# Performance work log

Hardware: AMD Instinct MI355X
Metric: run time of the kernel (lower is better)

Reference implementation:

```python
import jax, jax.numpy as jnp
import numpy as np

B = 32768
MAXD = 60               # max raw feature dim (user)
DIMS = [60, 51, 43]     # user, event, space
H = 256                 # HIDDEN_DIM
E = 256                 # EMBED_DIM
NH = 4                  # num heads
HD = H // NH            # head dim = 64
SCALE = float(np.sqrt(HD))
EPS = 1e-5


def setup_inputs() -> dict:
    key = jax.random.key(0)
    ks = iter(jax.random.split(key, 64))
    def rn(shape, scale=0.05):
        return jax.random.normal(next(ks), shape, dtype=jnp.float32) * scale
    inp = {}
    inp["anchor_feats"] = jax.random.normal(next(ks), (B, MAXD), dtype=jnp.float32)
    inp["item_feats"] = jax.random.normal(next(ks), (B, MAXD), dtype=jnp.float32)
    inp["anchor_type_ids"] = jax.random.randint(next(ks), (B,), 0, 3, dtype=jnp.int32)
    inp["item_type_ids"] = jax.random.randint(next(ks), (B,), 0, 3, dtype=jnp.int32)
    # per-type encoder MLPs; W1 zero-padded beyond each type's input dim (matches torch slicing x[:, :dim])
    W1 = rn((3, MAXD, H))
    row_mask = np.zeros((3, MAXD, 1), dtype=np.float32)
    for t, d in enumerate(DIMS):
        row_mask[t, :d, 0] = 1.0
    inp["enc_W1"] = W1 * jnp.asarray(row_mask)
    inp["enc_b1"] = rn((3, H)); inp["enc_g1"] = jnp.ones((3, H)); inp["enc_be1"] = jnp.zeros((3, H))
    inp["enc_W2"] = rn((3, H, H))
    inp["enc_b2"] = rn((3, H)); inp["enc_g2"] = jnp.ones((3, H)); inp["enc_be2"] = jnp.zeros((3, H))
    # two stacked HGT layers; 9 edge types (src*3+dst), 3 node types
    inp["hgt_Wk"] = rn((2, 9, H, H)); inp["hgt_Wq"] = rn((2, 9, H, H)); inp["hgt_Wv"] = rn((2, 9, H, H))
    inp["hgt_Wout"] = rn((2, 3, H, H))
    inp["hgt_g"] = jnp.ones((2, 3, H)); inp["hgt_b"] = jnp.zeros((2, 3, H))
    inp["out_W"] = rn((H, E)); inp["out_b"] = rn((E,))
    inp["out_g"] = jnp.ones((E,)); inp["out_be"] = jnp.zeros((E,))
    return inp


def _ln(x, g, b):
    m = x.mean(-1, keepdims=True)
    v = ((x - m) ** 2).mean(-1, keepdims=True)
    return (x - m) / jnp.sqrt(v + EPS) * g + b


def _encode(feats, tids, W1, b1, g1, be1, W2, b2, g2, be2):
    # per-type 2-layer MLP (Linear->LN->ReLU x2, dropout=eval noop), masked select
    h = jnp.zeros((feats.shape[0], H), feats.dtype)
    for t in range(3):
        z = jax.nn.relu(_ln(feats @ W1[t] + b1[t], g1[t], be1[t]))
        z = jax.nn.relu(_ln(z @ W2[t] + b2[t], g2[t], be2[t]))
        h = jnp.where((tids == t)[:, None], z, h)
    return h


def _hgt_apply(Wk, Wq, Wv, Wout, g, b, e, dt, src_h, dst_h):
    # single-dim dot-product attention per head, sigmoid gate
    Bn = src_h.shape[0]
    k = (src_h @ Wk[e]).reshape(Bn, NH, HD)
    q = (dst_h @ Wq[e]).reshape(Bn, NH, HD)
    v = (src_h @ Wv[e]).reshape(Bn, NH, HD)
    attn = jax.nn.sigmoid((q * k).sum(-1, keepdims=True) / SCALE)
    msg = (attn * v).reshape(Bn, H)
    return _ln(dst_h + msg @ Wout[dt], g[dt], b[dt])


def _hgt_hop(Wk, Wq, Wv, Wout, g, b, ha, hi, atid, itid):
    # torch code: ha_out from clone of ha, hi updated per disjoint (atype,itype) mask,
    # both updates read ORIGINAL ha/hi for each masked element
    ha_new, hi_new = ha, hi
    for a in range(3):
        for i in range(3):
            mask = ((atid == a) & (itid == i))[:, None]
            ua = _hgt_apply(Wk, Wq, Wv, Wout, g, b, i * 3 + a, a, hi, ha)  # item -> anchor
            ui = _hgt_apply(Wk, Wq, Wv, Wout, g, b, a * 3 + i, i, ha, hi)  # anchor -> item
            ha_new = jnp.where(mask, ua, ha_new)
            hi_new = jnp.where(mask, ui, hi_new)
    return ha_new, hi_new


def _l2norm(x):
    return x / jnp.maximum(jnp.linalg.norm(x, axis=-1, keepdims=True), 1e-12)


def reference(anchor_feats, item_feats, anchor_type_ids, item_type_ids,
              enc_W1, enc_b1, enc_g1, enc_be1, enc_W2, enc_b2, enc_g2, enc_be2,
              hgt_Wk, hgt_Wq, hgt_Wv, hgt_Wout, hgt_g, hgt_b,
              out_W, out_b, out_g, out_be):
    ha = _encode(anchor_feats, anchor_type_ids, enc_W1, enc_b1, enc_g1, enc_be1, enc_W2, enc_b2, enc_g2, enc_be2)
    hi = _encode(item_feats, item_type_ids, enc_W1, enc_b1, enc_g1, enc_be1, enc_W2, enc_b2, enc_g2, enc_be2)
    for L in range(2):
        ha, hi = _hgt_hop(hgt_Wk[L], hgt_Wq[L], hgt_Wv[L], hgt_Wout[L], hgt_g[L], hgt_b[L],
                          ha, hi, anchor_type_ids, item_type_ids)
    anchor_emb = _l2norm(_ln(ha @ out_W + out_b, out_g, out_be))
    item_emb = _l2norm(_ln(hi @ out_W + out_b, out_g, out_be))
    return anchor_emb, item_emb
```

## Files before the change

### kernel.cpp

```cpp
#include <hip/hip_runtime.h>
#include <math.h>

#define BN   32768
#define MAXD 60
#define HDIM 256
#define TR   16
#define LDX  260

typedef __attribute__((ext_vector_type(4))) float f32x4;
typedef __attribute__((ext_vector_type(8))) short bf16x8;

#define MFMA(a, b, c) __builtin_amdgcn_mfma_f32_16x16x32_bf16(a, b, c, 0, 0, 0)

__device__ __forceinline__ unsigned short f2bf(float f) {
  union { float f; unsigned u; } v; v.f = f;
  unsigned r = v.u + 0x7FFF + ((v.u >> 16) & 1);
  return (unsigned short)(r >> 16);
}

template <int LDXE>
__device__ __forceinline__ bf16x8 ldsAx(const unsigned short* buf, int rf,
                                        int ks, int lane) {
  const int row = rf * 16 + (lane & 15);
  const int ko = ks * 32 + ((lane >> 4) << 3);
  return *(const bf16x8*)(buf + row * LDXE + ko);
}

template <int KS>
__device__ __forceinline__ bf16x8 fragB(const unsigned short* __restrict__ W,
                                        int cfw, int ks, int lane) {
  return *(const bf16x8*)(W + ((size_t)(cfw * KS + ks) << 9) + (lane << 3));
}

__device__ __forceinline__ float red16(float p) {
  p += __shfl_xor(p, 1); p += __shfl_xor(p, 2);
  p += __shfl_xor(p, 4); p += __shfl_xor(p, 8);
  return p;
}

__device__ __forceinline__ void cross_ln(float* redS, float* redQ,
                                         const float sums[2][4],
                                         const float sumq[2][4], int lane,
                                         int wid, float mo[2][4],
                                         float ro[2][4]) {
  __syncthreads();
  if ((lane & 15) == 0) {
    #pragma unroll
    for (int rf = 0; rf < 2; ++rf)
      #pragma unroll
      for (int rr = 0; rr < 4; ++rr) {
        const int row = rf * 16 + ((lane >> 4) << 2) + rr;
        redS[row * 4 + wid] = sums[rf][rr];
        redQ[row * 4 + wid] = sumq[rf][rr];
      }
  }
  __syncthreads();
  #pragma unroll
  for (int rf = 0; rf < 2; ++rf)
    #pragma unroll
    for (int rr = 0; rr < 4; ++rr) {
      const int row = rf * 16 + ((lane >> 4) << 2) + rr;
      float s = redS[row * 4] + redS[row * 4 + 1] + redS[row * 4 + 2] + redS[row * 4 + 3];
      float z = redQ[row * 4] + redQ[row * 4 + 1] + redQ[row * 4 + 2] + redQ[row * 4 + 3];
      float m = s * (1.0f / HDIM);
      mo[rf][rr] = m;
      ro[rf][rr] = rsqrtf(z * (1.0f / HDIM) - m * m + 1e-5f);
    }
}


__device__ __forceinline__ void row_reduce(float* red, const float acc[TR],
                                           float m[TR], float rs[TR], int j) {
  const int lane = j & 63, wv = j >> 6;
  __syncthreads();
  #pragma unroll
  for (int r = 0; r < TR; ++r) {
    float s = acc[r], q = acc[r] * acc[r];
    #pragma unroll
    for (int o = 32; o; o >>= 1) { s += __shfl_xor(s, o); q += __shfl_xor(q, o); }
    if (lane == 0) { red[r * 8 + wv * 2] = s; red[r * 8 + wv * 2 + 1] = q; }
  }
  __syncthreads();
  #pragma unroll
  for (int r = 0; r < TR; ++r) {
    float s = red[r * 8 + 0] + red[r * 8 + 2] + red[r * 8 + 4] + red[r * 8 + 6];
    float q = red[r * 8 + 1] + red[r * 8 + 3] + red[r * 8 + 5] + red[r * 8 + 7];
    float mean = s * (1.0f / HDIM);
    float var  = q * (1.0f / HDIM) - mean * mean;
    m[r]  = mean;
    rs[r] = rsqrtf(var + 1e-5f);
  }
}

template <int KD, int ST>
__device__ __forceinline__ void matvec_l(const float* __restrict__ W,
                                         const float* zz, float acc[TR], int j) {
  #pragma unroll 2
  for (int k = 0; k < KD; k += 4) {
    const float w0 = W[(k + 0) * HDIM + j];
    const float w1 = W[(k + 1) * HDIM + j];
    const float w2 = W[(k + 2) * HDIM + j];
    const float w3 = W[(k + 3) * HDIM + j];
    #pragma unroll
    for (int r = 0; r < TR; ++r) {
      const float4 x = *(const float4*)(zz + r * ST + k);
      acc[r] = fmaf(x.w, w3, fmaf(x.z, w2, fmaf(x.y, w1, fmaf(x.x, w0, acc[r]))));
    }
  }
}


__global__ __launch_bounds__(256) void bucket_kernel(
    const int* __restrict__ atid, const int* __restrict__ itid,
    int* cnts, int* idxA, int* idxI, int* idxC) {
  __shared__ int lcnt[15], lbase[15];
  const int tid = threadIdx.x;
  const int r = blockIdx.x * 256 + tid;
  if (tid < 15) lcnt[tid] = 0;
  __syncthreads();
  const int a = atid[r], i = itid[r];
  const int c = a * 3 + i;
// ... 100 lines not shown
    const int col = (wid << 6) + (cf << 4) + (lane & 15);
    cb[cf] = b1[t * HDIM + col]; cg[cf] = g1[t * HDIM + col]; cbe[cf] = be1[t * HDIM + col];
  }
  float sums[2][4] = {}, sumq[2][4] = {};
  #pragma unroll
  for (int rf = 0; rf < 2; ++rf)
    #pragma unroll
    for (int cf = 0; cf < 4; ++cf)
      #pragma unroll
      for (int rr = 0; rr < 4; ++rr) {
        float x = acc[rf][cf][rr] + cb[cf];
        acc[rf][cf][rr] = x;
        sums[rf][rr] += x; sumq[rf][rr] += x * x;
      }
  #pragma unroll
  for (int rf = 0; rf < 2; ++rf)
    #pragma unroll
    for (int rr = 0; rr < 4; ++rr) { sums[rf][rr] = red16(sums[rf][rr]); sumq[rf][rr] = red16(sumq[rf][rr]); }
  float m[2][4], rs[2][4];
  cross_ln(sm.redS, sm.redQ, sums, sumq, lane, wid, m, rs);
  #pragma unroll
  for (int rf = 0; rf < 2; ++rf)
    #pragma unroll
    for (int cf = 0; cf < 4; ++cf) {
      const int col = (wid << 6) + (cf << 4) + (lane & 15);
      #pragma unroll
      for (int rr = 0; rr < 4; ++rr) {
        const int row = rf * 16 + ((lane >> 4) << 2) + rr;
        float zz = fmaxf((acc[rf][cf][rr] - m[rf][rr]) * rs[rf][rr] * cg[cf] + cbe[cf], 0.0f);
        sm.z[row * LDX + col] = f2bf(zz);
      }
    }
  __syncthreads();

  #pragma unroll
  for (int rf = 0; rf < 2; ++rf)
    #pragma unroll
    for (int cf = 0; cf < 4; ++cf) acc[rf][cf] = (f32x4){0.f, 0.f, 0.f, 0.f};
  #pragma unroll 2
  for (int ks = 0; ks < 8; ++ks) {
    bf16x8 a0 = ldsAx<LDX>(sm.z, 0, ks, lane);
    bf16x8 a1 = ldsAx<LDX>(sm.z, 1, ks, lane);
    #pragma unroll
    for (int cf = 0; cf < 4; ++cf) {
      bf16x8 w = fragB<8>(pW2 + (size_t)t * 65536, (wid << 2) + cf, ks, lane);
      acc[0][cf] = MFMA(a0, w, acc[0][cf]);
      acc[1][cf] = MFMA(a1, w, acc[1][cf]);
    }
  }
  #pragma unroll
  for (int cf = 0; cf < 4; ++cf) {
    const int col = (wid << 6) + (cf << 4) + (lane & 15);
    cb[cf] = b2[t * HDIM + col]; cg[cf] = g2[t * HDIM + col]; cbe[cf] = be2[t * HDIM + col];
  }
  float sums2[2][4] = {}, sumq2[2][4] = {};
  #pragma unroll
  for (int rf = 0; rf < 2; ++rf)
    #pragma unroll
    for (int cf = 0; cf < 4; ++cf)
      #pragma unroll
      for (int rr = 0; rr < 4; ++rr) {
        float x = acc[rf][cf][rr] + cb[cf];
        acc[rf][cf][rr] = x;
        sums2[rf][rr] += x; sumq2[rf][rr] += x * x;
      }
  #pragma unroll
  for (int rf = 0; rf < 2; ++rf)
    #pragma unroll
    for (int rr = 0; rr < 4; ++rr) { sums2[rf][rr] = red16(sums2[rf][rr]); sumq2[rf][rr] = red16(sumq2[rf][rr]); }
  cross_ln(sm.redS, sm.redQ, sums2, sumq2, lane, wid, m, rs);
  #pragma unroll
  for (int rf = 0; rf < 2; ++rf)
    #pragma unroll
    for (int cf = 0; cf < 4; ++cf) {
      const int col = (wid << 6) + (cf << 4) + (lane & 15);
      #pragma unroll
      for (int rr = 0; rr < 4; ++rr)
        hout[(size_t)mg[rf * 4 + rr] * HDIM + col] =
            fmaxf((acc[rf][cf][rr] - m[rf][rr]) * rs[rf][rr] * cg[cf] + cbe[cf], 0.0f);
    }
}


struct HopSmem {
  unsigned short xa[32 * LDX];
  unsigned short xi[32 * LDX];
  unsigned short msg[32 * LDX];
  float redS[128];
  float redQ[128];
  int rowsL[32];
};

__device__ __forceinline__ void hop_dir(
    const unsigned short* __restrict__ bq, const unsigned short* __restrict__ bk,
    const unsigned short* __restrict__ bv, const unsigned short* __restrict__ bo,
    const float* __restrict__ gg, const float* __restrict__ bb,
    const unsigned short* xdst, const unsigned short* xsrc,
    const float* __restrict__ hdst_g, float* __restrict__ hout_g,
    HopSmem& sm, const int mg[8], int lane, int wid) {
  f32x4 q[2][4] = {}; f32x4 kk[2][4] = {};
  #pragma unroll 2
  for (int ks = 0; ks < 8; ++ks) {
    bf16x8 ad0 = ldsAx<LDX>(xdst, 0, ks, lane), ad1 = ldsAx<LDX>(xdst, 1, ks, lane);
    bf16x8 as0 = ldsAx<LDX>(xsrc, 0, ks, lane), as1 = ldsAx<LDX>(xsrc, 1, ks, lane);
    #pragma unroll
    for (int cf = 0; cf < 4; ++cf) {
      bf16x8 wq = fragB<8>(bq, (wid << 2) + cf, ks, lane);
      bf16x8 wk = fragB<8>(bk, (wid << 2) + cf, ks, lane);
      q[0][cf]  = MFMA(ad0, wq, q[0][cf]);
      q[1][cf]  = MFMA(ad1, wq, q[1][cf]);
      kk[0][cf] = MFMA(as0, wk, kk[0][cf]);
      kk[1][cf] = MFMA(as1, wk, kk[1][cf]);
    }
  }
  float at[2][4];
  #pragma unroll
  for (int rf = 0; rf < 2; ++rf)
    #pragma unroll
    for (int rr = 0; rr < 4; ++rr) {
      float p = q[rf][0][rr] * kk[rf][0][rr] + q[rf][1][rr] * kk[rf][1][rr]
              + q[rf][2][rr] * kk[rf][2][rr] + q[rf][3][rr] * kk[rf][3][rr];
      p = red16(p);
      at[rf][rr] = 1.0f / (1.0f + __expf(-p * 0.125f));
    }
  f32x4 vv[2][4] = {};
  #pragma unroll 2
  for (int ks = 0; ks < 8; ++ks) {
    bf16x8 as0 = ldsAx<LDX>(xsrc, 0, ks, lane), as1 = ldsAx<LDX>(xsrc, 1, ks, lane);
    #pragma unroll
    for (int cf = 0; cf < 4; ++cf) {
      bf16x8 wv = fragB<8>(bv, (wid << 2) + cf, ks, lane);
      vv[0][cf] = MFMA(as0, wv, vv[0][cf]);
      vv[1][cf] = MFMA(as1, wv, vv[1][cf]);
    }
  }
  __syncthreads();
  #pragma unroll
  for (int rf = 0; rf < 2; ++rf)
    #pragma unroll
    for (int cf = 0; cf < 4; ++cf) {
      const int col = (wid << 6) + (cf << 4) + (lane & 15);
      #pragma unroll
      for (int rr = 0; rr < 4; ++rr) {
        const int row = rf * 16 + ((lane >> 4) << 2) + rr;
        sm.msg[row * LDX + col] = f2bf(vv[rf][cf][rr] * at[rf][rr]);
      }
    }
  __syncthreads();
  f32x4 oo[2][4] = {};
  #pragma unroll 2
  for (int ks = 0; ks < 8; ++ks) {
    bf16x8 am0 = ldsAx<LDX>(sm.msg, 0, ks, lane), am1 = ldsAx<LDX>(sm.msg, 1, ks, lane);
    #pragma unroll
    for (int cf = 0; cf < 4; ++cf) {
      bf16x8 wo = fragB<8>(bo, (wid << 2) + cf, ks, lane);
      oo[0][cf] = MFMA(am0, wo, oo[0][cf]);
      oo[1][cf] = MFMA(am1, wo, oo[1][cf]);
    }
  }
  float sums[2][4] = {}, sumq[2][4] = {};
  #pragma unroll
  for (int rf = 0; rf < 2; ++rf)
    #pragma unroll
    for (int cf = 0; cf < 4; ++cf) {
      const int col = (wid << 6) + (cf << 4) + (lane & 15);
      #pragma unroll
      for (int rr = 0; rr < 4; ++rr) {
        float x = hdst_g[(size_t)mg[rf * 4 + rr] * HDIM + col] + oo[rf][cf][rr];
        oo[rf][cf][rr] = x;
        sums[rf][rr] += x;
        sumq[rf][rr] += x * x;
      }
    }
  #pragma unroll
  for (int rf = 0; rf < 2; ++rf)
    #pragma unroll
    for (int rr = 0; rr < 4; ++rr) { sums[rf][rr] = red16(sums[rf][rr]); sumq[rf][rr] = red16(sumq[rf][rr]); }
  float m[2][4], rs[2][4];
  cross_ln(sm.redS, sm.redQ, sums, sumq, lane, wid, m, rs);
  float g4[4], b4[4];
  #pragma unroll
  for (int cf = 0; cf < 4; ++cf) {
    const int col = (wid << 6) + (cf << 4) + (lane & 15);
    g4[cf] = gg[col]; b4[cf] = bb[col];
  }
  #pragma unroll
  for (int rf = 0; rf < 2; ++rf)
    #pragma unroll
    for (int rr = 0; rr < 4; ++rr) {
      #pragma unroll
      for (int cf = 0; cf < 4; ++cf) {
        const int col = (wid << 6) + (cf << 4) + (lane & 15);
        hout_g[(size_t)mg[rf * 4 + rr] * HDIM + col] =
            (oo[rf][cf][rr] - m[rf][rr]) * rs[rf][rr] * g4[cf] + b4[cf];
      }
    }
}

__global__ __launch_bounds__(256) void hop_mfma_kernel(
    const unsigned short* __restrict__ bWk, const unsigned short* __restrict__ bWq,
    const unsigned short* __restrict__ bWv, const unsigned short* __restrict__ bWo,
    const float* __restrict__ g, const float* __restrict__ b,
    const int* __restrict__ idxC, const int* __restrict__ cnts,
    float* __restrict__ ha, float* __restrict__ hi) {
  const int l = blockIdx.x;
  int c, rb;
  if (l < 8192) { c = l & 7; rb = l >> 3; }
  else          { c = 8;     rb = l - 8192; }
  const int cnt = cnts[6 + c];
  const int base = rb * 32;
  if (base >= cnt) return;
  const int a = c / 3, i = c % 3;
  __shared__ HopSmem sm;
  const int tid = threadIdx.x;
  const int lane = tid & 63, wid = tid >> 6;

  if (tid < 32) {
    int rr = base + tid; if (rr > cnt - 1) rr = cnt - 1;
    sm.rowsL[tid] = idxC[c * BN + rr];
  }
  __syncthreads();
  const int cp = (tid & 127) * 2, rh = tid >> 7;
  #pragma unroll 4
  for (int r0 = 0; r0 < 32; r0 += 2) {
    const int r = r0 + rh;
    const size_t gb = (size_t)sm.rowsL[r] * HDIM + cp;
    float2 va = *(const float2*)(ha + gb);
    float2 vi = *(const float2*)(hi + gb);
    *(unsigned*)(sm.xa + r * LDX + cp) =
        (unsigned)f2bf(va.x) | ((unsigned)f2bf(va.y) << 16);
    *(unsigned*)(sm.xi + r * LDX + cp) =
        (unsigned)f2bf(vi.x) | ((unsigned)f2bf(vi.y) << 16);
  }
  int mg[8];
  #pragma unroll
  for (int rf = 0; rf < 2; ++rf)
    #pragma unroll
    for (int rr = 0; rr < 4; ++rr)
      mg[rf * 4 + rr] = sm.rowsL[rf * 16 + ((lane >> 4) << 2) + rr];
  __syncthreads();

  const size_t MS = (size_t)HDIM * HDIM;
  const int e1 = i * 3 + a;
  const int e2 = a * 3 + i;
  hop_dir(bWq + e1 * MS, bWk + e1 * MS, bWv + e1 * MS, bWo + a * MS,
          g + a * HDIM, b + a * HDIM, sm.xa, sm.xi, ha, ha, sm, mg, lane, wid);
  hop_dir(bWq + e2 * MS, bWk + e2 * MS, bWv + e2 * MS, bWo + i * MS,
          g + i * HDIM, b + i * HDIM, sm.xi, sm.xa, hi, hi, sm, mg, lane, wid);
}


struct OutSmem {
  unsigned short x[32 * LDX];
  float redS[128];
  float redQ[128];
};

__global__ __launch_bounds__(256) void out_mfma_kernel(
    const unsigned short* __restrict__ pW, const float* __restrict__ bb,
    const float* __restrict__ g, const float* __restrict__ be,
    float* __restrict__ out) {
  const int ent = blockIdx.y;
  const int base = blockIdx.x * 32;
  float* hsrc = out + (size_t)ent * BN * HDIM;
  __shared__ OutSmem sm;
  const int tid = threadIdx.x, lane = tid & 63, wid = tid >> 6;
  const int cp = (tid & 127) * 2, rh = tid >> 7;
  #pragma unroll 4
  for (int r0 = 0; r0 < 32; r0 += 2) {
    const int r = r0 + rh;
    const float2 v = *(const float2*)(hsrc + (size_t)(base + r) * HDIM + cp);
    *(unsigned*)(sm.x + r * LDX + cp) =
        (unsigned)f2bf(v.x) | ((unsigned)f2bf(v.y) << 16);
  }
  __syncthreads();
  f32x4 acc[2][4] = {};
  #pragma unroll 2
  for (int ks = 0; ks < 8; ++ks) {
    bf16x8 a0 = ldsAx<LDX>(sm.x, 0, ks, lane);
    bf16x8 a1 = ldsAx<LDX>(sm.x, 1, ks, lane);
    #pragma unroll
    for (int cf = 0; cf < 4; ++cf) {
      bf16x8 w = fragB<8>(pW, (wid << 2) + cf, ks, lane);
      acc[0][cf] = MFMA(a0, w, acc[0][cf]);
      acc[1][cf] = MFMA(a1, w, acc[1][cf]);
    }
  }
  float cb[4], cg[4], cbe[4];
  #pragma unroll
  for (int cf = 0; cf < 4; ++cf) {
    const int col = (wid << 6) + (cf << 4) + (lane & 15);
    cb[cf] = bb[col]; cg[cf] = g[col]; cbe[cf] = be[col];
  }
  float sums[2][4] = {}, sumq[2][4] = {};
  #pragma unroll
  for (int rf = 0; rf < 2; ++rf)
    #pragma unroll
    for (int cf = 0; cf < 4; ++cf)
      #pragma unroll
      for (int rr = 0; rr < 4; ++rr) {
        float x = acc[rf][cf][rr] + cb[cf];
        acc[rf][cf][rr] = x;
        sums[rf][rr] += x; sumq[rf][rr] += x * x;
      }
  #pragma unroll
  for (int rf = 0; rf < 2; ++rf)
    #pragma unroll
    for (int rr = 0; rr < 4; ++rr) { sums[rf][rr] = red16(sums[rf][rr]); sumq[rf][rr] = red16(sumq[rf][rr]); }
  float m[2][4], rs[2][4];
  cross_ln(sm.redS, sm.redQ, sums, sumq, lane, wid, m, rs);
  float s2[2][4] = {};
  #pragma unroll
  for (int rf = 0; rf < 2; ++rf)
    #pragma unroll
    for (int cf = 0; cf < 4; ++cf)
      #pragma unroll
      for (int rr = 0; rr < 4; ++rr) {
        float y = (acc[rf][cf][rr] - m[rf][rr]) * rs[rf][rr] * cg[cf] + cbe[cf];
        acc[rf][cf][rr] = y;
        s2[rf][rr] += y * y;
      }
  #pragma unroll
  for (int rf = 0; rf < 2; ++rf)
    #pragma unroll
    for (int rr = 0; rr < 4; ++rr) s2[rf][rr] = red16(s2[rf][rr]);
  __syncthreads();
  if ((lane & 15) == 0) {
    #pragma unroll
    for (int rf = 0; rf < 2; ++rf)
      #pragma unroll
      for (int rr = 0; rr < 4; ++rr) {
// ... 185 lines not shown
  float y[TR];
  #pragma unroll
  for (int r = 0; r < TR; ++r) y[r] = (acc[r] - m[r]) * rs[r] * gj + bej;
  const int lane = j & 63, wv = j >> 6;
  __syncthreads();
  #pragma unroll
  for (int r = 0; r < TR; ++r) {
    float p = y[r] * y[r];
    #pragma unroll
    for (int o = 32; o; o >>= 1) p += __shfl_xor(p, o);
    if (lane == 0) red[r * 4 + wv] = p;
  }
  __syncthreads();
  #pragma unroll
  for (int r = 0; r < TR; ++r) {
    float ss = red[r * 4] + red[r * 4 + 1] + red[r * 4 + 2] + red[r * 4 + 3];
    float inv = 1.0f / fmaxf(sqrtf(ss), 1e-12f);
    hsrc[(size_t)(base + r) * HDIM + j] = y[r] * inv;
  }
}


extern "C" void kernel_launch(void* const* d_in, const int* in_sizes, int n_in,
                              void* d_out, int out_size, void* d_ws,
                              size_t ws_size, hipStream_t stream) {
  const float* af   = (const float*)d_in[0];
  const float* itf  = (const float*)d_in[1];
  const int*   atid = (const int*)d_in[2];
  const int*   itid = (const int*)d_in[3];
  const float* eW1  = (const float*)d_in[4];
  const float* eb1  = (const float*)d_in[5];
  const float* eg1  = (const float*)d_in[6];
  const float* ebe1 = (const float*)d_in[7];
  const float* eW2  = (const float*)d_in[8];
  const float* eb2  = (const float*)d_in[9];
  const float* eg2  = (const float*)d_in[10];
  const float* ebe2 = (const float*)d_in[11];
  const float* hWk  = (const float*)d_in[12];
  const float* hWq  = (const float*)d_in[13];
  const float* hWv  = (const float*)d_in[14];
  const float* hWo  = (const float*)d_in[15];
  const float* hg   = (const float*)d_in[16];
  const float* hb   = (const float*)d_in[17];
  const float* oW   = (const float*)d_in[18];
  const float* ob   = (const float*)d_in[19];
  const float* og   = (const float*)d_in[20];
  const float* obe  = (const float*)d_in[21];

  float* out = (float*)d_out;
  float* ha = out;
  float* hi = out + (size_t)BN * HDIM;

  int* cnts = (int*)d_ws;
  int* idxA = cnts + 16;
  int* idxI = idxA + 3 * BN;
  int* idxC = idxI + 3 * BN;
  unsigned short* pW1 = (unsigned short*)(idxC + 9 * BN);
  unsigned short* pW2 = pW1 + 3 * 16384;
  unsigned short* pWk = pW2 + 3 * 65536;
  unsigned short* pWq = pWk + 18 * 65536;
  unsigned short* pWv = pWq + 18 * 65536;
  unsigned short* pWo = pWv + 18 * 65536;
  unsigned short* pOW = pWo + 6 * 65536;
  const size_t ws_need = (size_t)(16 + 15 * BN) * 4 +
                         ((size_t)3 * 16384 + (size_t)64 * 65536) * 2;
  const bool use_mfma = ws_size >= ws_need;

  hipMemsetAsync(cnts, 0, 16 * sizeof(int), stream);
  bucket_kernel<<<BN / 256, 256, 0, stream>>>(atid, itid, cnts, idxA, idxI, idxC);

  if (use_mfma) {
    wpack_kernel<<<3 * 16384 / 256, 256, 0, stream>>>(eW1, pW1, 3, 2, 60);
    wpack_kernel<<<3 * 65536 / 256, 256, 0, stream>>>(eW2, pW2, 3, 8, 256);
    wpack_kernel<<<18 * 65536 / 256, 256, 0, stream>>>(hWk, pWk, 18, 8, 256);
    wpack_kernel<<<18 * 65536 / 256, 256, 0, stream>>>(hWq, pWq, 18, 8, 256);
    wpack_kernel<<<18 * 65536 / 256, 256, 0, stream>>>(hWv, pWv, 18, 8, 256);
    wpack_kernel<<<6 * 65536 / 256, 256, 0, stream>>>(hWo, pWo, 6, 8, 256);
    wpack_kernel<<<65536 / 256, 256, 0, stream>>>(oW, pOW, 1, 8, 256);

    enc_mfma_kernel<<<dim3(BN / 32, 3, 2), 256, 0, stream>>>(
        af, itf, idxA, idxI, cnts, pW1, pW2,
        eb1, eg1, ebe1, eb2, eg2, ebe2, ha, hi);
    for (int L = 0; L < 2; ++L) {
      hop_mfma_kernel<<<9216, 256, 0, stream>>>(
          pWk + (size_t)L * 9 * 65536, pWq + (size_t)L * 9 * 65536,
          pWv + (size_t)L * 9 * 65536, pWo + (size_t)L * 3 * 65536,
          hg + L * 3 * HDIM, hb + L * 3 * HDIM, idxC, cnts, ha, hi);
    }
    out_mfma_kernel<<<dim3(BN / 32, 2), 256, 0, stream>>>(pOW, ob, og, obe, out);
  } else {
    enc_kernel<<<dim3((BN + TR - 1) / TR, 3, 2), 256, 0, stream>>>(
        af, itf, idxA, idxI, cnts, eW1, eb1, eg1, ebe1, eW2, eb2, eg2, ebe2,
        ha, hi);
    for (int L = 0; L < 2; ++L) {
      hop_kernel<<<dim3((BN + TR - 1) / TR, 9), 256, 0, stream>>>(
          hWk + (size_t)L * 9 * HDIM * HDIM, hWq + (size_t)L * 9 * HDIM * HDIM,
          hWv + (size_t)L * 9 * HDIM * HDIM, hWo + (size_t)L * 3 * HDIM * HDIM,
          hg + L * 3 * HDIM, hb + L * 3 * HDIM, idxC, cnts, ha, hi);
    }
    out_kernel<<<dim3(BN / TR, 2), 256, 0, stream>>>(oW, ob, og, obe, out);
  }
}
```

Before: 360.0 us.

## Process 64 rows per hop block and reuse two shared buffers for both directions

The HGT hop kernel now handles 64 gathered rows per block instead of 32, so every weight fragment loaded from global memory feeds four MFMA row tiles instead of two. The two directions' Q/K attention and V projections are computed before the output projections, so the input buffers can be overwritten with messages, cutting shared memory to two 64-row buffers. The gather loads now use float4 with 64-bit LDS stores. In exchange, register pressure rises (accumulators for 4x4 fragments plus a live V accumulator across phases, launch bounds of 2), and the grid is shaped (BN/64, 9), which launches many early-exiting blocks.

```diff
diff --git a/kernel.cpp b/kernel.cpp
--- a/kernel.cpp
+++ b/kernel.cpp
@@ -37,6 +37,7 @@
   p += __shfl_xor(p, 4); p += __shfl_xor(p, 8);
   return p;
 }
+
 
 __device__ __forceinline__ void cross_ln(float* redS, float* redQ,
                                          const float sums[2][4],
@@ -303,102 +304,113 @@
 }
 
 
-struct HopSmem {
-  unsigned short xa[32 * LDX];
-  unsigned short xi[32 * LDX];
-  unsigned short msg[32 * LDX];
-  float redS[128];
-  float redQ[128];
-  int rowsL[32];
+struct Hop64Smem {
+  unsigned short b0[64 * LDX];
+  unsigned short b1[64 * LDX];
+  float redS[256];
+  float redQ[256];
+  int rowsL[64];
 };
 
-__device__ __forceinline__ void hop_dir(
+__device__ __forceinline__ void cross_ln64(float* redS, float* redQ,
+                                           const float sums[4][4],
+                                           const float sumq[4][4], int lane,
+                                           int wid, float mo[4][4],
+                                           float ro[4][4]) {
+  __syncthreads();
+  if ((lane & 15) == 0) {
+    #pragma unroll
+    for (int rf = 0; rf < 4; ++rf)
+      #pragma unroll
+      for (int rr = 0; rr < 4; ++rr) {
+        const int row = rf * 16 + ((lane >> 4) << 2) + rr;
+        redS[row * 4 + wid] = sums[rf][rr];
+        redQ[row * 4 + wid] = sumq[rf][rr];
+      }
+  }
+  __syncthreads();
+  #pragma unroll
+  for (int rf = 0; rf < 4; ++rf)
+    #pragma unroll
+    for (int rr = 0; rr < 4; ++rr) {
+      const int row = rf * 16 + ((lane >> 4) << 2) + rr;
+      float s = redS[row * 4] + redS[row * 4 + 1] + redS[row * 4 + 2] + redS[row * 4 + 3];
+      float z = redQ[row * 4] + redQ[row * 4 + 1] + redQ[row * 4 + 2] + redQ[row * 4 + 3];
+      float m = s * (1.0f / HDIM);
+      mo[rf][rr] = m;
+      ro[rf][rr] = rsqrtf(z * (1.0f / HDIM) - m * m + 1e-5f);
+    }
+}
+
+__device__ __forceinline__ void qk_attn64(
     const unsigned short* __restrict__ bq, const unsigned short* __restrict__ bk,
-    const unsigned short* __restrict__ bv, const unsigned short* __restrict__ bo,
+    const unsigned short* D, const unsigned short* S, float at[4][4],
+    int lane, int wid) {
+  float p[4][4] = {};
+  #pragma unroll
+  for (int cf = 0; cf < 4; ++cf) {
+    f32x4 qt[4] = {}, kt[4] = {};
+    #pragma unroll
+    for (int ks = 0; ks < 8; ++ks) {
+      bf16x8 wq = fragB<8>(bq, (wid << 2) + cf, ks, lane);
+      bf16x8 wk = fragB<8>(bk, (wid << 2) + cf, ks, lane);
+      #pragma unroll
+      for (int rf = 0; rf < 4; ++rf) {
+        qt[rf] = MFMA(ldsAx<LDX>(D, rf, ks, lane), wq, qt[rf]);
+        kt[rf] = MFMA(ldsAx<LDX>(S, rf, ks, lane), wk, kt[rf]);
+      }
+    }
+    #pragma unroll
+    for (int rf = 0; rf < 4; ++rf)
+      #pragma unroll
+      for (int rr = 0; rr < 4; ++rr)
+        p[rf][rr] = fmaf(qt[rf][rr], kt[rf][rr], p[rf][rr]);
+  }
+  #pragma unroll
+  for (int rf = 0; rf < 4; ++rf)
+    #pragma unroll
+    for (int rr = 0; rr < 4; ++rr)
+      at[rf][rr] = 1.0f / (1.0f + __expf(-red16(p[rf][rr]) * 0.125f));
+}
+
+__device__ __forceinline__ void o_ln_write64(
+    const unsigned short* msgb, const unsigned short* __restrict__ bo,
+    const float* __restrict__ resid, float* __restrict__ outp,
     const float* __restrict__ gg, const float* __restrict__ bb,
-    const unsigned short* xdst, const unsigned short* xsrc,
-    const float* __restrict__ hdst_g, float* __restrict__ hout_g,
-    HopSmem& sm, const int mg[8], int lane, int wid) {
-  f32x4 q[2][4] = {}; f32x4 kk[2][4] = {};
+    Hop64Smem& sm, const int mg[16], int lane, int wid) {
+  f32x4 oo[4][4] = {};
   #pragma unroll 2
   for (int ks = 0; ks < 8; ++ks) {
-    bf16x8 ad0 = ldsAx<LDX>(xdst, 0, ks, lane), ad1 = ldsAx<LDX>(xdst, 1, ks, lane);
-    bf16x8 as0 = ldsAx<LDX>(xsrc, 0, ks, lane), as1 = ldsAx<LDX>(xsrc, 1, ks, lane);
+    bf16x8 af[4];
+    #pragma unroll
+    for (int rf = 0; rf < 4; ++rf) af[rf] = ldsAx<LDX>(msgb, rf, ks, lane);
     #pragma unroll
     for (int cf = 0; cf < 4; ++cf) {
-      bf16x8 wq = fragB<8>(bq, (wid << 2) + cf, ks, lane);
-      bf16x8 wk = fragB<8>(bk, (wid << 2) + cf, ks, lane);
-      q[0][cf]  = MFMA(ad0, wq, q[0][cf]);
-      q[1][cf]  = MFMA(ad1, wq, q[1][cf]);
-      kk[0][cf] = MFMA(as0, wk, kk[0][cf]);
-      kk[1][cf] = MFMA(as1, wk, kk[1][cf]);
-    }
-  }
-  float at[2][4];
-  #pragma unroll
-  for (int rf = 0; rf < 2; ++rf)
-    #pragma unroll
-    for (int rr = 0; rr < 4; ++rr) {
-      float p = q[rf][0][rr] * kk[rf][0][rr] + q[rf][1][rr] * kk[rf][1][rr]
-              + q[rf][2][rr] * kk[rf][2][rr] + q[rf][3][rr] * kk[rf][3][rr];
-      p = red16(p);
-      at[rf][rr] = 1.0f / (1.0f + __expf(-p * 0.125f));
-    }
-  f32x4 vv[2][4] = {};
-  #pragma unroll 2
-  for (int ks = 0; ks < 8; ++ks) {
-    bf16x8 as0 = ldsAx<LDX>(xsrc, 0, ks, lane), as1 = ldsAx<LDX>(xsrc, 1, ks, lane);
-    #pragma unroll
-    for (int cf = 0; cf < 4; ++cf) {
-      bf16x8 wv = fragB<8>(bv, (wid << 2) + cf, ks, lane);
-      vv[0][cf] = MFMA(as0, wv, vv[0][cf]);
-      vv[1][cf] = MFMA(as1, wv, vv[1][cf]);
-    }
-  }
-  __syncthreads();
-  #pragma unroll
-  for (int rf = 0; rf < 2; ++rf)
+      bf16x8 wo = fragB<8>(bo, (wid << 2) + cf, ks, lane);
+      #pragma unroll
+      for (int rf = 0; rf < 4; ++rf) oo[rf][cf] = MFMA(af[rf], wo, oo[rf][cf]);
+    }
+  }
+  float sums[4][4] = {}, sumq[4][4] = {};
+  #pragma unroll
+  for (int rf = 0; rf < 4; ++rf)
     #pragma unroll
     for (int cf = 0; cf < 4; ++cf) {
       const int col = (wid << 6) + (cf << 4) + (lane & 15);
       #pragma unroll
       for (int rr = 0; rr < 4; ++rr) {
-        const int row = rf * 16 + ((lane >> 4) << 2) + rr;
-        sm.msg[row * LDX + col] = f2bf(vv[rf][cf][rr] * at[rf][rr]);
-      }
-    }
-  __syncthreads();
-  f32x4 oo[2][4] = {};
-  #pragma unroll 2
-  for (int ks = 0; ks < 8; ++ks) {
-    bf16x8 am0 = ldsAx<LDX>(sm.msg, 0, ks, lane), am1 = ldsAx<LDX>(sm.msg, 1, ks, lane);
-    #pragma unroll
-    for (int cf = 0; cf < 4; ++cf) {
-      bf16x8 wo = fragB<8>(bo, (wid << 2) + cf, ks, lane);
-      oo[0][cf] = MFMA(am0, wo, oo[0][cf]);
-      oo[1][cf] = MFMA(am1, wo, oo[1][cf]);
-    }
-  }
-  float sums[2][4] = {}, sumq[2][4] = {};
-  #pragma unroll
-  for (int rf = 0; rf < 2; ++rf)
-    #pragma unroll
-    for (int cf = 0; cf < 4; ++cf) {
-      const int col = (wid << 6) + (cf << 4) + (lane & 15);
-      #pragma unroll
-      for (int rr = 0; rr < 4; ++rr) {
-        float x = hdst_g[(size_t)mg[rf * 4 + rr] * HDIM + col] + oo[rf][cf][rr];
+        float x = resid[(size_t)mg[rf * 4 + rr] * HDIM + col] + oo[rf][cf][rr];
         oo[rf][cf][rr] = x;
         sums[rf][rr] += x;
         sumq[rf][rr] += x * x;
       }
     }
   #pragma unroll
-  for (int rf = 0; rf < 2; ++rf)
+  for (int rf = 0; rf < 4; ++rf)
     #pragma unroll
     for (int rr = 0; rr < 4; ++rr) { sums[rf][rr] = red16(sums[rf][rr]); sumq[rf][rr] = red16(sumq[rf][rr]); }
-  float m[2][4], rs[2][4];
-  cross_ln(sm.redS, sm.redQ, sums, sumq, lane, wid, m, rs);
+  float m[4][4], rs[4][4];
+  cross_ln64(sm.redS, sm.redQ, sums, sumq, lane, wid, m, rs);
   float g4[4], b4[4];
   #pragma unroll
   for (int cf = 0; cf < 4; ++cf) {
@@ -406,56 +418,56 @@
     g4[cf] = gg[col]; b4[cf] = bb[col];
   }
   #pragma unroll
-  for (int rf = 0; rf < 2; ++rf)
-    #pragma unroll
-    for (int rr = 0; rr < 4; ++rr) {
+  for (int rf = 0; rf < 4; ++rf)
+    #pragma unroll
+    for (int rr = 0; rr < 4; ++rr)
       #pragma unroll
       for (int cf = 0; cf < 4; ++cf) {
         const int col = (wid << 6) + (cf << 4) + (lane & 15);
-        hout_g[(size_t)mg[rf * 4 + rr] * HDIM + col] =
+        outp[(size_t)mg[rf * 4 + rr] * HDIM + col] =
             (oo[rf][cf][rr] - m[rf][rr]) * rs[rf][rr] * g4[cf] + b4[cf];
       }
-    }
-}
-
-__global__ __launch_bounds__(256) void hop_mfma_kernel(
+}
+
+__global__ __launch_bounds__(256, 2) void hop64_kernel(
     const unsigned short* __restrict__ bWk, const unsigned short* __restrict__ bWq,
     const unsigned short* __restrict__ bWv, const unsigned short* __restrict__ bWo,
     const float* __restrict__ g, const float* __restrict__ b,
     const int* __restrict__ idxC, const int* __restrict__ cnts,
     float* __restrict__ ha, float* __restrict__ hi) {
-  const int l = blockIdx.x;
-  int c, rb;
-  if (l < 8192) { c = l & 7; rb = l >> 3; }
-  else          { c = 8;     rb = l - 8192; }
+  const int c = blockIdx.y, a = c / 3, i = c % 3;
   const int cnt = cnts[6 + c];
-  const int base = rb * 32;
+  const int base = blockIdx.x * 64;
   if (base >= cnt) return;
-  const int a = c / 3, i = c % 3;
-  __shared__ HopSmem sm;
-  const int tid = threadIdx.x;
-  const int lane = tid & 63, wid = tid >> 6;
-
-  if (tid < 32) {
+  __shared__ Hop64Smem sm;
+  const int tid = threadIdx.x, lane = tid & 63, wid = tid >> 6;
+
+  if (tid < 64) {
     int rr = base + tid; if (rr > cnt - 1) rr = cnt - 1;
     sm.rowsL[tid] = idxC[c * BN + rr];
   }
   __syncthreads();
-  const int cp = (tid & 127) * 2, rh = tid >> 7;
-  #pragma unroll 4
-  for (int r0 = 0; r0 < 32; r0 += 2) {
-    const int r = r0 + rh;
-    const size_t gb = (size_t)sm.rowsL[r] * HDIM + cp;
-    float2 va = *(const float2*)(ha + gb);
-    float2 vi = *(const float2*)(hi + gb);
-    *(unsigned*)(sm.xa + r * LDX + cp) =
-        (unsigned)f2bf(va.x) | ((unsigned)f2bf(va.y) << 16);
-    *(unsigned*)(sm.xi + r * LDX + cp) =
-        (unsigned)f2bf(vi.x) | ((unsigned)f2bf(vi.y) << 16);
-  }
-  int mg[8];
-  #pragma unroll
-  for (int rf = 0; rf < 2; ++rf)
+  {
+    const int cp4 = (tid & 63) * 4, rh = tid >> 6;
+    #pragma unroll 4
+    for (int r0 = 0; r0 < 64; r0 += 4) {
+      const int r = r0 + rh;
+      const size_t gb = (size_t)sm.rowsL[r] * HDIM + cp4;
+      const float4 va = *(const float4*)(ha + gb);
+      const float4 vi = *(const float4*)(hi + gb);
+      unsigned long long pa =
+          (unsigned long long)((unsigned)f2bf(va.x) | ((unsigned)f2bf(va.y) << 16)) |
+          ((unsigned long long)((unsigned)f2bf(va.z) | ((unsigned)f2bf(va.w) << 16)) << 32);
+      unsigned long long pi =
+          (unsigned long long)((unsigned)f2bf(vi.x) | ((unsigned)f2bf(vi.y) << 16)) |
+          ((unsigned long long)((unsigned)f2bf(vi.z) | ((unsigned)f2bf(vi.w) << 16)) << 32);
+      *(unsigned long long*)(sm.b0 + r * LDX + cp4) = pa;
+      *(unsigned long long*)(sm.b1 + r * LDX + cp4) = pi;
+    }
+  }
+  int mg[16];
+  #pragma unroll
+  for (int rf = 0; rf < 4; ++rf)
     #pragma unroll
     for (int rr = 0; rr < 4; ++rr)
       mg[rf * 4 + rr] = sm.rowsL[rf * 16 + ((lane >> 4) << 2) + rr];
@@ -464,10 +476,61 @@
   const size_t MS = (size_t)HDIM * HDIM;
   const int e1 = i * 3 + a;
   const int e2 = a * 3 + i;
-  hop_dir(bWq + e1 * MS, bWk + e1 * MS, bWv + e1 * MS, bWo + a * MS,
-          g + a * HDIM, b + a * HDIM, sm.xa, sm.xi, ha, ha, sm, mg, lane, wid);
-  hop_dir(bWq + e2 * MS, bWk + e2 * MS, bWv + e2 * MS, bWo + i * MS,
-          g + i * HDIM, b + i * HDIM, sm.xi, sm.xa, hi, hi, sm, mg, lane, wid);
+
+  float at0[4][4], at1[4][4];
+  qk_attn64(bWq + e1 * MS, bWk + e1 * MS, sm.b0, sm.b1, at0, lane, wid);
+  qk_attn64(bWq + e2 * MS, bWk + e2 * MS, sm.b1, sm.b0, at1, lane, wid);
+
+  f32x4 vv1[4][4] = {};
+  #pragma unroll 2
+  for (int ks = 0; ks < 8; ++ks) {
+    bf16x8 af[4];
+    #pragma unroll
+    for (int rf = 0; rf < 4; ++rf) af[rf] = ldsAx<LDX>(sm.b0, rf, ks, lane);
+    #pragma unroll
+    for (int cf = 0; cf < 4; ++cf) {
+      bf16x8 wv = fragB<8>(bWv + e2 * MS, (wid << 2) + cf, ks, lane);
+      #pragma unroll
+      for (int rf = 0; rf < 4; ++rf) vv1[rf][cf] = MFMA(af[rf], wv, vv1[rf][cf]);
+    }
+  }
+  __syncthreads();
+
+  #pragma unroll
+  for (int cf = 0; cf < 4; ++cf) {
+    f32x4 vt[4] = {};
+    #pragma unroll
+    for (int ks = 0; ks < 8; ++ks) {
+      bf16x8 wv = fragB<8>(bWv + e1 * MS, (wid << 2) + cf, ks, lane);
+      #pragma unroll
+      for (int rf = 0; rf < 4; ++rf)
+        vt[rf] = MFMA(ldsAx<LDX>(sm.b1, rf, ks, lane), wv, vt[rf]);
+    }
+    const int col = (wid << 6) + (cf << 4) + (lane & 15);
+    #pragma unroll
+    for (int rf = 0; rf < 4; ++rf)
+      #pragma unroll
+      for (int rr = 0; rr < 4; ++rr)
+        sm.b0[(rf * 16 + ((lane >> 4) << 2) + rr) * LDX + col] =
+            f2bf(vt[rf][rr] * at0[rf][rr]);
+  }
+  __syncthreads();
+
+  #pragma unroll
+  for (int cf = 0; cf < 4; ++cf) {
+    const int col = (wid << 6) + (cf << 4) + (lane & 15);
+    #pragma unroll
+    for (int rf = 0; rf < 4; ++rf)
+      #pragma unroll
+      for (int rr = 0; rr < 4; ++rr)
+        sm.b1[(rf * 16 + ((lane >> 4) << 2) + rr) * LDX + col] =
+            f2bf(vv1[rf][cf][rr] * at1[rf][rr]);
+  }
+
+  o_ln_write64(sm.b0, bWo + a * MS, ha, ha, g + a * HDIM, b + a * HDIM,
+               sm, mg, lane, wid);
+  o_ln_write64(sm.b1, bWo + i * MS, hi, hi, g + i * HDIM, b + i * HDIM,
+               sm, mg, lane, wid);
 }
 
 
@@ -819,7 +882,7 @@
         af, itf, idxA, idxI, cnts, pW1, pW2,
         eb1, eg1, ebe1, eb2, eg2, ebe2, ha, hi);
     for (int L = 0; L < 2; ++L) {
-      hop_mfma_kernel<<<9216, 256, 0, stream>>>(
+      hop64_kernel<<<dim3(BN / 64, 9), 256, 0, stream>>>(
           pWk + (size_t)L * 9 * 65536, pWq + (size_t)L * 9 * 65536,
           pWv + (size_t)L * 9 * 65536, pWo + (size_t)L * 3 * 65536,
           hg + L * 3 * HDIM, hb + L * 3 * HDIM, idxC, cnts, ha, hi);
```

New measurement: 638.1 us. 77.2% more time.

## Split hop kernel across eight waves with cross-wave attention reduction

Applied to the files above, without the earlier changes.

The HGT hop kernel now runs 512 threads per block: eight waves instead of four. Each wave computes half of one head's 64 output columns for Q, K, V and the output projection. Per-head attention dot products are combined across wave pairs through an LDS buffer, and the LayerNorm reduction is extended to eight partials. The launch becomes a 2D grid over row blocks and edge types. The aim is more waves in flight and fewer accumulator registers per wave, paid for with extra barriers and duplicated LDS reads of the input tiles.

```diff
diff --git a/kernel.cpp b/kernel.cpp
--- a/kernel.cpp
+++ b/kernel.cpp
@@ -303,78 +303,131 @@
 }
 
 
-struct HopSmem {
+struct Hop8Smem {
   unsigned short xa[32 * LDX];
   unsigned short xi[32 * LDX];
   unsigned short msg[32 * LDX];
-  float redS[128];
-  float redQ[128];
+  float attP[32 * 8];
+  float redS[32 * 8];
+  float redQ[32 * 8];
   int rowsL[32];
 };
 
-__device__ __forceinline__ void hop_dir(
+__device__ __forceinline__ void cross_ln8(float* redS, float* redQ,
+                                          const float sums[2][4],
+                                          const float sumq[2][4], int lane,
+                                          int wid, float mo[2][4],
+                                          float ro[2][4]) {
+  __syncthreads();
+  if ((lane & 15) == 0) {
+    #pragma unroll
+    for (int rf = 0; rf < 2; ++rf)
+      #pragma unroll
+      for (int rr = 0; rr < 4; ++rr) {
+        const int row = rf * 16 + ((lane >> 4) << 2) + rr;
+        redS[row * 8 + wid] = sums[rf][rr];
+        redQ[row * 8 + wid] = sumq[rf][rr];
+      }
+  }
+  __syncthreads();
+  #pragma unroll
+  for (int rf = 0; rf < 2; ++rf)
+    #pragma unroll
+    for (int rr = 0; rr < 4; ++rr) {
+      const int row = rf * 16 + ((lane >> 4) << 2) + rr;
+      float s = 0.0f, z = 0.0f;
+      #pragma unroll
+      for (int w = 0; w < 8; ++w) { s += redS[row * 8 + w]; z += redQ[row * 8 + w]; }
+      float m = s * (1.0f / HDIM);
+      mo[rf][rr] = m;
+      ro[rf][rr] = rsqrtf(z * (1.0f / HDIM) - m * m + 1e-5f);
+    }
+}
+
+__device__ __forceinline__ void hop_dir8(
     const unsigned short* __restrict__ bq, const unsigned short* __restrict__ bk,
     const unsigned short* __restrict__ bv, const unsigned short* __restrict__ bo,
     const float* __restrict__ gg, const float* __restrict__ bb,
     const unsigned short* xdst, const unsigned short* xsrc,
     const float* __restrict__ hdst_g, float* __restrict__ hout_g,
-    HopSmem& sm, const int mg[8], int lane, int wid) {
-  f32x4 q[2][4] = {}; f32x4 kk[2][4] = {};
+    Hop8Smem& sm, const int mg[8], int lane, int wid) {
+  const int hw = wid >> 1, ch = wid & 1;
+  const int cfw0 = (hw << 2) + (ch << 1);
+
+  f32x4 q[2][2] = {}; f32x4 kk[2][2] = {};
   #pragma unroll 2
   for (int ks = 0; ks < 8; ++ks) {
     bf16x8 ad0 = ldsAx<LDX>(xdst, 0, ks, lane), ad1 = ldsAx<LDX>(xdst, 1, ks, lane);
     bf16x8 as0 = ldsAx<LDX>(xsrc, 0, ks, lane), as1 = ldsAx<LDX>(xsrc, 1, ks, lane);
     #pragma unroll
-    for (int cf = 0; cf < 4; ++cf) {
-      bf16x8 wq = fragB<8>(bq, (wid << 2) + cf, ks, lane);
-      bf16x8 wk = fragB<8>(bk, (wid << 2) + cf, ks, lane);
+    for (int cf = 0; cf < 2; ++cf) {
+      bf16x8 wq = fragB<8>(bq, cfw0 + cf, ks, lane);
+      bf16x8 wk = fragB<8>(bk, cfw0 + cf, ks, lane);
       q[0][cf]  = MFMA(ad0, wq, q[0][cf]);
       q[1][cf]  = MFMA(ad1, wq, q[1][cf]);
       kk[0][cf] = MFMA(as0, wk, kk[0][cf]);
       kk[1][cf] = MFMA(as1, wk, kk[1][cf]);
     }
   }
+  float part[2][4];
+  #pragma unroll
+  for (int rf = 0; rf < 2; ++rf)
+    #pragma unroll
+    for (int rr = 0; rr < 4; ++rr) {
+      float p = q[rf][0][rr] * kk[rf][0][rr] + q[rf][1][rr] * kk[rf][1][rr];
+      part[rf][rr] = red16(p);
+    }
+  __syncthreads();
+  if ((lane & 15) == 0) {
+    #pragma unroll
+    for (int rf = 0; rf < 2; ++rf)
+      #pragma unroll
+      for (int rr = 0; rr < 4; ++rr) {
+        const int row = rf * 16 + ((lane >> 4) << 2) + rr;
+        sm.attP[row * 8 + wid] = part[rf][rr];
+      }
+  }
+  __syncthreads();
   float at[2][4];
   #pragma unroll
   for (int rf = 0; rf < 2; ++rf)
     #pragma unroll
     for (int rr = 0; rr < 4; ++rr) {
-      float p = q[rf][0][rr] * kk[rf][0][rr] + q[rf][1][rr] * kk[rf][1][rr]
-              + q[rf][2][rr] * kk[rf][2][rr] + q[rf][3][rr] * kk[rf][3][rr];
-      p = red16(p);
+      const int row = rf * 16 + ((lane >> 4) << 2) + rr;
+      float p = sm.attP[row * 8 + (hw << 1)] + sm.attP[row * 8 + (hw << 1) + 1];
       at[rf][rr] = 1.0f / (1.0f + __expf(-p * 0.125f));
     }
-  f32x4 vv[2][4] = {};
+  f32x4 vv[2][2] = {};
   #pragma unroll 2
   for (int ks = 0; ks < 8; ++ks) {
     bf16x8 as0 = ldsAx<LDX>(xsrc, 0, ks, lane), as1 = ldsAx<LDX>(xsrc, 1, ks, lane);
     #pragma unroll
-    for (int cf = 0; cf < 4; ++cf) {
-      bf16x8 wv = fragB<8>(bv, (wid << 2) + cf, ks, lane);
+    for (int cf = 0; cf < 2; ++cf) {
+      bf16x8 wv = fragB<8>(bv, cfw0 + cf, ks, lane);
       vv[0][cf] = MFMA(as0, wv, vv[0][cf]);
       vv[1][cf] = MFMA(as1, wv, vv[1][cf]);
     }
   }
   __syncthreads();
   #pragma unroll
-  for (int rf = 0; rf < 2; ++rf)
-    #pragma unroll
-    for (int cf = 0; cf < 4; ++cf) {
-      const int col = (wid << 6) + (cf << 4) + (lane & 15);
+  for (int cf = 0; cf < 2; ++cf) {
+    const int col = (hw << 6) + (ch << 5) + (cf << 4) + (lane & 15);
+    #pragma unroll
+    for (int rf = 0; rf < 2; ++rf)
       #pragma unroll
       for (int rr = 0; rr < 4; ++rr) {
         const int row = rf * 16 + ((lane >> 4) << 2) + rr;
         sm.msg[row * LDX + col] = f2bf(vv[rf][cf][rr] * at[rf][rr]);
       }
-    }
-  __syncthreads();
-  f32x4 oo[2][4] = {};
+  }
+  __syncthreads();
+  f32x4 oo[2][2] = {};
   #pragma unroll 2
   for (int ks = 0; ks < 8; ++ks) {
     bf16x8 am0 = ldsAx<LDX>(sm.msg, 0, ks, lane), am1 = ldsAx<LDX>(sm.msg, 1, ks, lane);
     #pragma unroll
-    for (int cf = 0; cf < 4; ++cf) {
-      bf16x8 wo = fragB<8>(bo, (wid << 2) + cf, ks, lane);
+    for (int cf = 0; cf < 2; ++cf) {
+      bf16x8 wo = fragB<8>(bo, cfw0 + cf, ks, lane);
       oo[0][cf] = MFMA(am0, wo, oo[0][cf]);
       oo[1][cf] = MFMA(am1, wo, oo[1][cf]);
     }
@@ -383,8 +436,8 @@
   #pragma unroll
   for (int rf = 0; rf < 2; ++rf)
     #pragma unroll
-    for (int cf = 0; cf < 4; ++cf) {
-      const int col = (wid << 6) + (cf << 4) + (lane & 15);
+    for (int cf = 0; cf < 2; ++cf) {
+      const int col = (hw << 6) + (ch << 5) + (cf << 4) + (lane & 15);
       #pragma unroll
       for (int rr = 0; rr < 4; ++rr) {
         float x = hdst_g[(size_t)mg[rf * 4 + rr] * HDIM + col] + oo[rf][cf][rr];
@@ -398,41 +451,37 @@
     #pragma unroll
     for (int rr = 0; rr < 4; ++rr) { sums[rf][rr] = red16(sums[rf][rr]); sumq[rf][rr] = red16(sumq[rf][rr]); }
   float m[2][4], rs[2][4];
-  cross_ln(sm.redS, sm.redQ, sums, sumq, lane, wid, m, rs);
-  float g4[4], b4[4];
-  #pragma unroll
-  for (int cf = 0; cf < 4; ++cf) {
-    const int col = (wid << 6) + (cf << 4) + (lane & 15);
-    g4[cf] = gg[col]; b4[cf] = bb[col];
+  cross_ln8(sm.redS, sm.redQ, sums, sumq, lane, wid, m, rs);
+  float g2[2], b2[2];
+  #pragma unroll
+  for (int cf = 0; cf < 2; ++cf) {
+    const int col = (hw << 6) + (ch << 5) + (cf << 4) + (lane & 15);
+    g2[cf] = gg[col]; b2[cf] = bb[col];
   }
   #pragma unroll
   for (int rf = 0; rf < 2; ++rf)
     #pragma unroll
     for (int rr = 0; rr < 4; ++rr) {
       #pragma unroll
-      for (int cf = 0; cf < 4; ++cf) {
-        const int col = (wid << 6) + (cf << 4) + (lane & 15);
+      for (int cf = 0; cf < 2; ++cf) {
+        const int col = (hw << 6) + (ch << 5) + (cf << 4) + (lane & 15);
         hout_g[(size_t)mg[rf * 4 + rr] * HDIM + col] =
-            (oo[rf][cf][rr] - m[rf][rr]) * rs[rf][rr] * g4[cf] + b4[cf];
-      }
-    }
-}
-
-__global__ __launch_bounds__(256) void hop_mfma_kernel(
+            (oo[rf][cf][rr] - m[rf][rr]) * rs[rf][rr] * g2[cf] + b2[cf];
+      }
+    }
+}
+
+__global__ __launch_bounds__(512) void hop_mfma_kernel(
     const unsigned short* __restrict__ bWk, const unsigned short* __restrict__ bWq,
     const unsigned short* __restrict__ bWv, const unsigned short* __restrict__ bWo,
     const float* __restrict__ g, const float* __restrict__ b,
     const int* __restrict__ idxC, const int* __restrict__ cnts,
     float* __restrict__ ha, float* __restrict__ hi) {
-  const int l = blockIdx.x;
-  int c, rb;
-  if (l < 8192) { c = l & 7; rb = l >> 3; }
-  else          { c = 8;     rb = l - 8192; }
+  const int c = blockIdx.y, a = c / 3, i = c % 3;
   const int cnt = cnts[6 + c];
-  const int base = rb * 32;
+  const int base = blockIdx.x * 32;
   if (base >= cnt) return;
-  const int a = c / 3, i = c % 3;
-  __shared__ HopSmem sm;
+  __shared__ Hop8Smem sm;
   const int tid = threadIdx.x;
   const int lane = tid & 63, wid = tid >> 6;
 
@@ -441,17 +490,19 @@
     sm.rowsL[tid] = idxC[c * BN + rr];
   }
   __syncthreads();
-  const int cp = (tid & 127) * 2, rh = tid >> 7;
-  #pragma unroll 4
-  for (int r0 = 0; r0 < 32; r0 += 2) {
-    const int r = r0 + rh;
-    const size_t gb = (size_t)sm.rowsL[r] * HDIM + cp;
-    float2 va = *(const float2*)(ha + gb);
-    float2 vi = *(const float2*)(hi + gb);
-    *(unsigned*)(sm.xa + r * LDX + cp) =
-        (unsigned)f2bf(va.x) | ((unsigned)f2bf(va.y) << 16);
-    *(unsigned*)(sm.xi + r * LDX + cp) =
-        (unsigned)f2bf(vi.x) | ((unsigned)f2bf(vi.y) << 16);
+  {
+    const int cp = (tid & 127) * 2, rh = tid >> 7;
+    #pragma unroll 4
+    for (int r0 = 0; r0 < 32; r0 += 4) {
+      const int r = r0 + rh;
+      const size_t gb = (size_t)sm.rowsL[r] * HDIM + cp;
+      float2 va = *(const float2*)(ha + gb);
+      float2 vi = *(const float2*)(hi + gb);
+      *(unsigned*)(sm.xa + r * LDX + cp) =
+          (unsigned)f2bf(va.x) | ((unsigned)f2bf(va.y) << 16);
+      *(unsigned*)(sm.xi + r * LDX + cp) =
+          (unsigned)f2bf(vi.x) | ((unsigned)f2bf(vi.y) << 16);
+    }
   }
   int mg[8];
   #pragma unroll
@@ -464,10 +515,10 @@
   const size_t MS = (size_t)HDIM * HDIM;
   const int e1 = i * 3 + a;
   const int e2 = a * 3 + i;
-  hop_dir(bWq + e1 * MS, bWk + e1 * MS, bWv + e1 * MS, bWo + a * MS,
-          g + a * HDIM, b + a * HDIM, sm.xa, sm.xi, ha, ha, sm, mg, lane, wid);
-  hop_dir(bWq + e2 * MS, bWk + e2 * MS, bWv + e2 * MS, bWo + i * MS,
-          g + i * HDIM, b + i * HDIM, sm.xi, sm.xa, hi, hi, sm, mg, lane, wid);
+  hop_dir8(bWq + e1 * MS, bWk + e1 * MS, bWv + e1 * MS, bWo + a * MS,
+           g + a * HDIM, b + a * HDIM, sm.xa, sm.xi, ha, ha, sm, mg, lane, wid);
+  hop_dir8(bWq + e2 * MS, bWk + e2 * MS, bWv + e2 * MS, bWo + i * MS,
+           g + i * HDIM, b + i * HDIM, sm.xi, sm.xa, hi, hi, sm, mg, lane, wid);
 }
 
 
@@ -819,7 +870,7 @@
         af, itf, idxA, idxI, cnts, pW1, pW2,
         eb1, eg1, ebe1, eb2, eg2, ebe2, ha, hi);
     for (int L = 0; L < 2; ++L) {
-      hop_mfma_kernel<<<9216, 256, 0, stream>>>(
+      hop_mfma_kernel<<<dim3(BN / 32, 9), 512, 0, stream>>>(
           pWk + (size_t)L * 9 * 65536, pWq + (size_t)L * 9 * 65536,
           pWv + (size_t)L * 9 * 65536, pWo + (size_t)L * 3 * 65536,
           hg + L * 3 * HDIM, hb + L * 3 * HDIM, idxC, cnts, ha, hi);
```

New measurement: 516.7 us. 43.5% more time.
